# Performance work log

Measured on AMD Instinct MI355X. Metric: run time of the kernel, lower is better.

The kernel has to match this reference:

```python
import jax, jax.numpy as jnp
import numpy as np
from jax import lax

# Hardcoded module constants (from source)
T, B = 8, 64
CIN, C, HW, NCLS = 3, 64, 32, 10
V_INIT, V_DECAY, V_THR = 0.0, 0.8, 1.2


def conv_raw(x, w, b):
    # x: [T, B, Cin, H, W] -> conv2d per timestep, stride 1, pad 1
    t, bsz = x.shape[:2]
    xf = x.reshape((t * bsz,) + x.shape[2:])
    y = lax.conv_general_dilated(
        xf, w, window_strides=(1, 1), padding=[(1, 1), (1, 1)],
        dimension_numbers=('NCHW', 'OIHW', 'NCHW'))
    y = y + b[None, :, None, None]
    return y.reshape((t, bsz) + y.shape[1:])


def lif(i_cur):
    # NOTE: original code reads v[t] from the v_init-initialized tensor each
    # step (not v[t-1]), so there is NO temporal recurrence: v = v_init*decay + I[t]
    v = V_INIT * V_DECAY + i_cur
    return (v >= V_THR).astype(i_cur.dtype)


def setup_inputs() -> dict:
    key = jax.random.key(0)
    ks = jax.random.split(key, 7)
    spike_input = jax.random.uniform(ks[0], (T, B, CIN, HW, HW), jnp.float32)
    # original uses plain torch.randn for weights and biases
    w1 = jax.random.normal(ks[1], (C, CIN, 3, 3), jnp.float32)
    b1 = jax.random.normal(ks[2], (C,), jnp.float32)
    w2 = jax.random.normal(ks[3], (C, C, 3, 3), jnp.float32)
    b2 = jax.random.normal(ks[4], (C,), jnp.float32)
    wfc = jax.random.normal(ks[5], (NCLS, C * HW * HW), jnp.float32)
    bfc = jax.random.normal(ks[6], (NCLS,), jnp.float32)
    return {"spike_input": spike_input, "w1": w1, "b1": b1,
            "w2": w2, "b2": b2, "wfc": wfc, "bfc": bfc}


def reference(spike_input, w1, b1, w2, b2, wfc, bfc):
    x = lif(conv_raw(spike_input, w1, b1))      # [T,B,64,32,32] binary spikes
    x = lif(conv_raw(x, w2, b2))                # [T,B,64,32,32]
    x = x.reshape(T, B, -1)                     # [T,B,64*32*32]
    out = jnp.einsum('tbi,oi->tbo', x, wfc) + bfc
    return out.sum(0)                           # [B, 10]
```

## Files before the change

### kernel.cpp

```cpp
#include <hip/hip_runtime.h>
#include <hip/hip_bf16.h>


typedef __attribute__((ext_vector_type(8))) short bf16x8;
typedef __attribute__((ext_vector_type(4))) float f32x4;
typedef __attribute__((ext_vector_type(4))) int   i32x4;

#define S1Q (5.5f/127.0f)
#define S2Q (S1Q/254.0f)

static const size_t SZ_IMG  = 65536;
static const size_t OFF_S8  = 0;
static const size_t OFF_CNT = 512*SZ_IMG;
static const size_t OFF_W1F = OFF_CNT + (4u<<20);
static const size_t OFF_BQ  = OFF_W1F + 8192;

#define SWZ(cp) (((cp) >> 1) & 3)

__device__ __forceinline__ void gl_lds16(const void* g, void* l) {
  __builtin_amdgcn_global_load_lds(
      (const __attribute__((address_space(1))) unsigned int*)g,
      (__attribute__((address_space(3))) unsigned int*)l, 16, 0, 0);
}

__global__ __launch_bounds__(256) void kprep(
    const float* __restrict__ w1, const float* __restrict__ w2,
    short* __restrict__ W1F, signed char* __restrict__ Bq, float* __restrict__ out)
{
  int i = blockIdx.x*256 + threadIdx.x;
  if (i < 640) out[i] = 0.f;
  if (i < 4096) {
    int t2 = i >> 11, r = i & 2047, co = r >> 5, k = r & 31;
    short o = 0;
    if (k < 27) {
      int s = k/3, ci = k - s*3;
      float w = w1[co*27 + ci*9 + s];
      __hip_bfloat16 h = __float2bfloat16(w);
      if (t2 == 0) o = *(short*)&h;
      else { __hip_bfloat16 lo = __float2bfloat16(w - (float)h); o = *(short*)&lo; }
    }
    W1F[i] = o;
  }
  if (i < 36864) {
    int co = i/576, rem = i - co*576, ci = rem/9, s = rem - ci*9;
    float w = w2[i];
    int q1 = (int)roundf(w * (1.0f/S1Q)); q1 = q1 > 127 ? 127 : (q1 < -127 ? -127 : q1);
    float r1 = w - S1Q*(float)q1;
    int q2 = (int)roundf(r1 * (1.0f/S2Q)); q2 = q2 > 127 ? 127 : (q2 < -127 ? -127 : q2);
    int off = s*4096 + co*64 + ci;
    Bq[off] = (signed char)q1; Bq[36864 + off] = (signed char)q2;
  }
}

__global__ __launch_bounds__(256, 4) void conv1_k(
    const float* __restrict__ x, const short* __restrict__ W1F,
    const float* __restrict__ b1, unsigned char* __restrict__ S8)
{
  const int j   = blockIdx.x;
  const int img = j & 511, rh = j >> 9;
  const int tid = threadIdx.x;
  const int w   = tid >> 6;
  const int l   = tid & 63;
  const int lm  = l & 15, lk = l >> 4;

  __shared__ int xt4[1944];
  __shared__ i32x4 bnc4[4][16][4];
  unsigned short* xs = (unsigned short*)xt4;
  unsigned char*  bnc = (unsigned char*)bnc4;

  for (int i = tid; i < 1944; i += 256) xt4[i] = 0;
  __syncthreads();
  const float* xin = x + (size_t)img * 3072;
  for (int jj = tid; jj < 1728; jj += 256) {
    int ci = jj / 576, rem = jj - ci*576, rl = rem >> 5, c = rem & 31;
    int gr = rh*16 - 1 + rl;
    float f = (gr >= 0 && gr < 32) ? xin[ci*1024 + gr*32 + c] : 0.f;
    __hip_bfloat16 h = __float2bfloat16(f);
    __hip_bfloat16 lo = __float2bfloat16(f - (float)h);
    int idx = ci*648 + rl*36 + (c+1);
    xs[idx] = *(unsigned short*)&h;
    xs[idx + 1944] = *(unsigned short*)&lo;
  }
  __syncthreads();

  bf16x8 Wf[2][4];
  float  b1v[4];
  #pragma unroll
  for (int t2 = 0; t2 < 2; t2++)
    #pragma unroll
    for (int nf = 0; nf < 4; nf++)
      Wf[t2][nf] = *(const bf16x8*)(W1F + t2*2048 + (nf*16+lm)*32 + lk*8);
  #pragma unroll
  for (int nf = 0; nf < 4; nf++) b1v[nf] = b1[nf*16 + lm];

  int off16[8];
  #pragma unroll
  for (int e = 0; e < 8; e++) {
    int k = lk*8 + e;
    if (k < 27) { int s = k/3, ci = k - s*3, dr = s/3, dc = s - dr*3;
                  off16[e] = ci*648 + dr*36 + dc; }
    else off16[e] = 0;
  }

  unsigned char* S8b = S8 + (size_t)img * SZ_IMG;
  for (int fi = 0; fi < 8; fi++) {
    const int pxF = w*8 + fi;
    const int lrow = pxF >> 1, colh = pxF & 1;
    const int base16 = lrow*36 + colh*16 + lm;
    bf16x8 ah, al;
    #pragma unroll
    for (int e = 0; e < 8; e++) {
      int idx = base16 + off16[e];
      ah[e] = (short)xs[idx];
      al[e] = (short)xs[idx + 1944];
    }
    f32x4 acc[4] = {};
    #pragma unroll
    for (int nf = 0; nf < 4; nf++) {
      acc[nf] = __builtin_amdgcn_mfma_f32_16x16x32_bf16(ah, Wf[0][nf], acc[nf], 0,0,0);
      acc[nf] = __builtin_amdgcn_mfma_f32_16x16x32_bf16(al, Wf[0][nf], acc[nf], 0,0,0);
      acc[nf] = __builtin_amdgcn_mfma_f32_16x16x32_bf16(ah, Wf[1][nf], acc[nf], 0,0,0);
      acc[nf] = __builtin_amdgcn_mfma_f32_16x16x32_bf16(al, Wf[1][nf], acc[nf], 0,0,0);
    }
    #pragma unroll
    for (int nf = 0; nf < 4; nf++)
      #pragma unroll
      for (int e4 = 0; e4 < 4; e4++) {
        float v = acc[nf][e4] + b1v[nf];
        bnc[w*1024 + (lk*4+e4)*64 + nf*16 + lm] = (v >= 1.2f) ? 1 : 0;
      }
    const int pxl = l >> 2, coq = l & 3;
    i32x4 sp = *(const i32x4*)(bnc + w*1024 + pxl*64 + coq*16);
    const int gcol = colh*16 + pxl;
    const int grow = rh*16 + lrow;
    const int cq = coq ^ SWZ(gcol + 1);
    *(i32x4*)(S8b + (size_t)(grow*32 + gcol)*64 + cq*16) = sp;
  }
}

__global__ __launch_bounds__(512, 2) void conv2_k(
    const unsigned char* __restrict__ S8, const signed char* __restrict__ Bq,
    const float* __restrict__ b2, unsigned char* __restrict__ cnt)
{
  extern __shared__ __align__(16) unsigned char lds[];
  unsigned char* Abuf = lds;
  unsigned char* Blds = lds + 43520;

  const int j  = blockIdx.x;
  const int b  = j & 63;
  const int rs = (j >> 6) & 3;
  const int ch = j >> 8;
  const int tid = threadIdx.x;
  const int wv = tid >> 6, l = tid & 63;
  const int lm = l & 15, lk = l >> 4;
  const int rp = wv >> 1;
  const int cq = wv & 1;
  const int colocal = cq*16 + lm;

  const float b2v = b2[ch*32 + colocal];

  {
    i32x4 z = {0,0,0,0};
    i32x4* ap = (i32x4*)Abuf;
    for (int c = tid; c < 2720; c += 512) ap[c] = z;
  }
  __syncthreads();

  {
    const signed char* Bsrc = Bq;
    #pragma unroll
    for (int it = 0; it < 5; it++) {
      const int c = it*512 + tid;
      if (c < 2304) {
        const int q = c / 1152, r = c - q*1152, s = r >> 7, r2 = r & 127;
        const int col = r2 >> 2, cic = r2 & 3;
        gl_lds16(Bsrc + q*36864 + s*4096 + (ch*32+col)*64 + cic*16, Blds + c*16);
      }
    }
    const unsigned char* Simg = S8 + (size_t)b*SZ_IMG;
    #pragma unroll
    for (int it = 0; it < 3; it++) {
      const int c = it*512 + tid;
      if (c < 1280) {
        const int row = c >> 7, grow = rs*8 - 1 + row;
        if (grow >= 0 && grow < 32)
          gl_lds16(Simg + grow*2048 + (c&127)*16, Abuf + row*2176 + 64 + (c&127)*16);
      }
    }
  }
  __syncthreads();

  unsigned int cntp[4] = {};

  for (int t = 0; t < 8; t++) {
    if (t < 7) {
      const unsigned char* Simg = S8 + (size_t)((t+1)*64 + b)*SZ_IMG;
      unsigned char* bufn = Abuf + ((t+1) & 1)*21760;
      #pragma unroll
      for (int it = 0; it < 3; it++) {
        const int c = it*512 + tid;
        if (c < 1280) {
          const int row = c >> 7, grow = rs*8 - 1 + row;
          if (grow >= 0 && grow < 32)
            gl_lds16(Simg + grow*2048 + (c&127)*16, bufn + row*2176 + 64 + (c&127)*16);
        }
      }
    }

    const unsigned char* ab = Abuf + (t & 1)*21760;
    i32x4 acc1[4] = {}, acc2[4] = {};
    __builtin_amdgcn_s_setprio(1);
    #pragma unroll
    for (int s = 0; s < 9; s++) {
      const int dr = s/3, dc = s - dr*3;
      i32x4 Bf1 = *(const i32x4*)(Blds + s*2048 + colocal*64 + lk*16);
      i32x4 Bf2 = *(const i32x4*)(Blds + 18432 + s*2048 + colocal*64 + lk*16);
      #pragma unroll
      for (int a = 0; a < 4; a++) {
        const int lr = rp*2 + (a>>1) + dr;
        const int cp = ((a&1)<<4) + lm + dc;
        i32x4 Af = *(const i32x4*)(ab + lr*2176 + cp*64 + ((lk ^ SWZ(cp)) << 4));
        acc1[a] = __builtin_amdgcn_mfma_i32_16x16x64_i8(Af, Bf1, acc1[a], 0,0,0);
        acc2[a] = __builtin_amdgcn_mfma_i32_16x16x64_i8(Af, Bf2, acc2[a], 0,0,0);
      }
    }
    __builtin_amdgcn_s_setprio(0);

    #pragma unroll
    for (int a = 0; a < 4; a++) {
      unsigned int p = 0;
      #pragma unroll
      for (int e = 0; e < 4; e++) {
        float v = S1Q*(float)acc1[a][e] + S2Q*(float)acc2[a][e] + b2v;
        p |= (v >= 1.2f ? 1u : 0u) << (8*e);
      }
      cntp[a] += p;
    }
    __syncthreads();
  }

  unsigned int* bb = (unsigned int*)Abuf;
  #pragma unroll
  for (int a = 0; a < 4; a++) {
    const int lrow = rp*2 + (a>>1);
    const int u = lrow*8 + (a&1)*4 + lk;
    bb[colocal*64 + (((u>>2) ^ (colocal & 15)) << 2) + (u&3)] = cntp[a];
  }
  __syncthreads();
  {
    const int co = tid >> 4, tc = tid & 15;
    i32x4 v = *(const i32x4*)(bb + co*64 + (tc << 2));
    const int g = tc ^ (co & 15);
    *(i32x4*)(cnt + (size_t)(b*64 + ch*32 + co)*1024 + rs*256 + g*16) = v;
  }
}

__global__ __launch_bounds__(256) void fc_k(
    const unsigned char* __restrict__ cnt, const float* __restrict__ wfc,
    const float* __restrict__ bfc, float* __restrict__ out)
{
  const int ig = blockIdx.x & 63;
  const int bg = blockIdx.x >> 6;
  const int tid = threadIdx.x;
  const int w = tid >> 6, l = tid & 63;
  const int b0 = bg*8 + w*2;

  float acc[2][10] = {};
  #pragma unroll
  for (int k = 0; k < 4; k++) {
    const int i4 = ig*256 + k*64 + l;
    float4 wv[10];
    #pragma unroll
    for (int o = 0; o < 10; o++)
      wv[o] = *(const float4*)(wfc + (size_t)o*65536 + (size_t)i4*4);
    #pragma unroll
    for (int bb = 0; bb < 2; bb++) {
      uchar4 cv = *(const uchar4*)(cnt + (size_t)(b0+bb)*65536 + (size_t)i4*4);
      float c0 = cv.x, c1 = cv.y, c2 = cv.z, c3 = cv.w;
      #pragma unroll
      for (int o = 0; o < 10; o++)
        acc[bb][o] += wv[o].x*c0 + wv[o].y*c1 + wv[o].z*c2 + wv[o].w*c3;
    }
  }
  #pragma unroll
  for (int bb = 0; bb < 2; bb++)
    #pragma unroll
    for (int o = 0; o < 10; o++) {
      float v = acc[bb][o];
      for (int off = 32; off > 0; off >>= 1) v += __shfl_down(v, off, 64);
      acc[bb][o] = v;
    }
  if (l == 0) {
    #pragma unroll
    for (int bb = 0; bb < 2; bb++)
      #pragma unroll
      for (int o = 0; o < 10; o++) {
        float v = acc[bb][o];
        if (ig == 0) v += 8.0f * bfc[o];
        atomicAdd(out + (b0+bb)*10 + o, v);
      }
  }
}

extern "C" void kernel_launch(void* const* d_in, const int* in_sizes, int n_in,
                              void* d_out, int out_size, void* d_ws, size_t ws_size,
                              hipStream_t stream)
{
  const float* x   = (const float*)d_in[0];
  const float* w1  = (const float*)d_in[1];
  const float* b1  = (const float*)d_in[2];
  const float* w2  = (const float*)d_in[3];
  const float* b2  = (const float*)d_in[4];
  const float* wfc = (const float*)d_in[5];
  const float* bfc = (const float*)d_in[6];
  float* out = (float*)d_out;

  unsigned char* ws  = (unsigned char*)d_ws;
  unsigned char* S8  = ws + OFF_S8;
  unsigned char* cnt = ws + OFF_CNT;
  short*         W1F = (short*)(ws + OFF_W1F);
  signed char*   Bq  = (signed char*)(ws + OFF_BQ);

  kprep<<<144, 256, 0, stream>>>(w1, w2, W1F, Bq, out);
  conv1_k<<<1024, 256, 0, stream>>>(x, W1F, b1, S8);
  conv2_k<<<512, 512, 80384, stream>>>(S8, Bq, b2, cnt);
  fc_k<<<512, 256, 0, stream>>>(cnt, wfc, bfc, out);
}
```

Measured before the change: 146.1 us.

## Fuse FC into conv2 epilogue and compute conv1 weight split in-kernel

The FC layer is folded into the conv2 kernel's epilogue. Each block multiplies its spike-count tile by the matching wfc slice, reduces through shuffles and LDS, and atomically adds into the output, so the cnt buffer round trip and the separate fc launch go away. The conv1 bf16 hi/lo weight split now happens inside conv1 instead of in the prep kernel, and the bias is written into out during prep. In exchange, wfc is re-read per block with less batch reuse and there are more atomics per output element.

New measurement: 136.2 us. -6.7%, faster.

```diff
diff --git a/kernel.cpp b/kernel.cpp
--- a/kernel.cpp
+++ b/kernel.cpp
@@ -11,9 +11,7 @@
 
 static const size_t SZ_IMG  = 65536;
 static const size_t OFF_S8  = 0;
-static const size_t OFF_CNT = 512*SZ_IMG;
-static const size_t OFF_W1F = OFF_CNT + (4u<<20);
-static const size_t OFF_BQ  = OFF_W1F + 8192;
+static const size_t OFF_BQ  = 512*SZ_IMG;
 
 #define SWZ(cp) (((cp) >> 1) & 3)
 
@@ -24,23 +22,11 @@
 }
 
 __global__ __launch_bounds__(256) void kprep(
-    const float* __restrict__ w1, const float* __restrict__ w2,
-    short* __restrict__ W1F, signed char* __restrict__ Bq, float* __restrict__ out)
+    const float* __restrict__ w2, const float* __restrict__ bfc,
+    signed char* __restrict__ Bq, float* __restrict__ out)
 {
   int i = blockIdx.x*256 + threadIdx.x;
-  if (i < 640) out[i] = 0.f;
-  if (i < 4096) {
-    int t2 = i >> 11, r = i & 2047, co = r >> 5, k = r & 31;
-    short o = 0;
-    if (k < 27) {
-      int s = k/3, ci = k - s*3;
-      float w = w1[co*27 + ci*9 + s];
-      __hip_bfloat16 h = __float2bfloat16(w);
-      if (t2 == 0) o = *(short*)&h;
-      else { __hip_bfloat16 lo = __float2bfloat16(w - (float)h); o = *(short*)&lo; }
-    }
-    W1F[i] = o;
-  }
+  if (i < 640) out[i] = 8.0f * bfc[i % 10];
   if (i < 36864) {
     int co = i/576, rem = i - co*576, ci = rem/9, s = rem - ci*9;
     float w = w2[i];
@@ -53,7 +39,7 @@
 }
 
 __global__ __launch_bounds__(256, 4) void conv1_k(
-    const float* __restrict__ x, const short* __restrict__ W1F,
+    const float* __restrict__ x, const float* __restrict__ w1,
     const float* __restrict__ b1, unsigned char* __restrict__ S8)
 {
   const int j   = blockIdx.x;
@@ -81,26 +67,28 @@
     xs[idx] = *(unsigned short*)&h;
     xs[idx + 1944] = *(unsigned short*)&lo;
   }
-  __syncthreads();
 
   bf16x8 Wf[2][4];
   float  b1v[4];
-  #pragma unroll
-  for (int t2 = 0; t2 < 2; t2++)
-    #pragma unroll
-    for (int nf = 0; nf < 4; nf++)
-      Wf[t2][nf] = *(const bf16x8*)(W1F + t2*2048 + (nf*16+lm)*32 + lk*8);
-  #pragma unroll
-  for (int nf = 0; nf < 4; nf++) b1v[nf] = b1[nf*16 + lm];
-
   int off16[8];
   #pragma unroll
   for (int e = 0; e < 8; e++) {
     int k = lk*8 + e;
-    if (k < 27) { int s = k/3, ci = k - s*3, dr = s/3, dc = s - dr*3;
-                  off16[e] = ci*648 + dr*36 + dc; }
+    int s = k/3, ci = k - s*3;
+    if (k < 27) { int dr = s/3, dc = s - dr*3; off16[e] = ci*648 + dr*36 + dc; }
     else off16[e] = 0;
-  }
+    #pragma unroll
+    for (int nf = 0; nf < 4; nf++) {
+      float wv = (k < 27) ? w1[(nf*16+lm)*27 + ci*9 + s] : 0.f;
+      __hip_bfloat16 h = __float2bfloat16(wv);
+      __hip_bfloat16 lo = __float2bfloat16(wv - (float)h);
+      Wf[0][nf][e] = *(short*)&h;
+      Wf[1][nf][e] = *(short*)&lo;
+    }
+  }
+  #pragma unroll
+  for (int nf = 0; nf < 4; nf++) b1v[nf] = b1[nf*16 + lm];
+  __syncthreads();
 
   unsigned char* S8b = S8 + (size_t)img * SZ_IMG;
   for (int fi = 0; fi < 8; fi++) {
@@ -138,9 +126,10 @@
   }
 }
 
-__global__ __launch_bounds__(512, 2) void conv2_k(
+__global__ __launch_bounds__(512, 2) void conv2fc_k(
     const unsigned char* __restrict__ S8, const signed char* __restrict__ Bq,
-    const float* __restrict__ b2, unsigned char* __restrict__ cnt)
+    const float* __restrict__ b2, const float* __restrict__ wfc,
+    float* __restrict__ out)
 {
   extern __shared__ __align__(16) unsigned char lds[];
   unsigned char* Abuf = lds;
@@ -247,58 +236,44 @@
     bb[colocal*64 + (((u>>2) ^ (colocal & 15)) << 2) + (u&3)] = cntp[a];
   }
   __syncthreads();
+
+  float facc[10];
   {
-    const int co = tid >> 4, tc = tid & 15;
-    i32x4 v = *(const i32x4*)(bb + co*64 + (tc << 2));
-    const int g = tc ^ (co & 15);
-    *(i32x4*)(cnt + (size_t)(b*64 + ch*32 + co)*1024 + rs*256 + g*16) = v;
-  }
-}
-
-__global__ __launch_bounds__(256) void fc_k(
-    const unsigned char* __restrict__ cnt, const float* __restrict__ wfc,
-    const float* __restrict__ bfc, float* __restrict__ out)
-{
-  const int ig = blockIdx.x & 63;
-  const int bg = blockIdx.x >> 6;
-  const int tid = threadIdx.x;
-  const int w = tid >> 6, l = tid & 63;
-  const int b0 = bg*8 + w*2;
-
-  float acc[2][10] = {};
+    const int co = tid >> 4, seg = tid & 15;
+    i32x4 cw = *(const i32x4*)(bb + co*64 + ((seg ^ (co & 15)) << 2));
+    const unsigned char* cb = (const unsigned char*)&cw;
+    const size_t ibase = (size_t)(ch*32 + co)*1024 + rs*256 + seg*16;
+    #pragma unroll
+    for (int o = 0; o < 10; o++) {
+      const float* wp = wfc + (size_t)o*65536 + ibase;
+      float s0 = 0.f;
+      #pragma unroll
+      for (int q4 = 0; q4 < 4; q4++) {
+        float4 wv4 = *(const float4*)(wp + q4*4);
+        s0 += wv4.x*(float)cb[q4*4+0] + wv4.y*(float)cb[q4*4+1]
+            + wv4.z*(float)cb[q4*4+2] + wv4.w*(float)cb[q4*4+3];
+      }
+      facc[o] = s0;
+    }
+  }
   #pragma unroll
-  for (int k = 0; k < 4; k++) {
-    const int i4 = ig*256 + k*64 + l;
-    float4 wv[10];
-    #pragma unroll
-    for (int o = 0; o < 10; o++)
-      wv[o] = *(const float4*)(wfc + (size_t)o*65536 + (size_t)i4*4);
-    #pragma unroll
-    for (int bb = 0; bb < 2; bb++) {
-      uchar4 cv = *(const uchar4*)(cnt + (size_t)(b0+bb)*65536 + (size_t)i4*4);
-      float c0 = cv.x, c1 = cv.y, c2 = cv.z, c3 = cv.w;
-      #pragma unroll
-      for (int o = 0; o < 10; o++)
-        acc[bb][o] += wv[o].x*c0 + wv[o].y*c1 + wv[o].z*c2 + wv[o].w*c3;
-    }
-  }
-  #pragma unroll
-  for (int bb = 0; bb < 2; bb++)
-    #pragma unroll
-    for (int o = 0; o < 10; o++) {
-      float v = acc[bb][o];
-      for (int off = 32; off > 0; off >>= 1) v += __shfl_down(v, off, 64);
-      acc[bb][o] = v;
-    }
+  for (int o = 0; o < 10; o++) {
+    float v = facc[o];
+    #pragma unroll
+    for (int off = 32; off > 0; off >>= 1) v += __shfl_down(v, off, 64);
+    facc[o] = v;
+  }
+  float* red = (float*)(Abuf + 16384);
   if (l == 0) {
     #pragma unroll
-    for (int bb = 0; bb < 2; bb++)
-      #pragma unroll
-      for (int o = 0; o < 10; o++) {
-        float v = acc[bb][o];
-        if (ig == 0) v += 8.0f * bfc[o];
-        atomicAdd(out + (b0+bb)*10 + o, v);
-      }
+    for (int o = 0; o < 10; o++) red[wv*10 + o] = facc[o];
+  }
+  __syncthreads();
+  if (tid < 10) {
+    float v = 0.f;
+    #pragma unroll
+    for (int q = 0; q < 8; q++) v += red[q*10 + tid];
+    atomicAdd(out + b*10 + tid, v);
   }
 }
 
@@ -317,12 +292,9 @@
 
   unsigned char* ws  = (unsigned char*)d_ws;
   unsigned char* S8  = ws + OFF_S8;
-  unsigned char* cnt = ws + OFF_CNT;
-  short*         W1F = (short*)(ws + OFF_W1F);
   signed char*   Bq  = (signed char*)(ws + OFF_BQ);
 
-  kprep<<<144, 256, 0, stream>>>(w1, w2, W1F, Bq, out);
-  conv1_k<<<1024, 256, 0, stream>>>(x, W1F, b1, S8);
-  conv2_k<<<512, 512, 80384, stream>>>(S8, Bq, b2, cnt);
-  fc_k<<<512, 256, 0, stream>>>(cnt, wfc, bfc, out);
-}
+  kprep<<<144, 256, 0, stream>>>(w2, bfc, Bq, out);
+  conv1_k<<<1024, 256, 0, stream>>>(x, w1, b1, S8);
+  conv2fc_k<<<512, 512, 80384, stream>>>(S8, Bq, b2, wfc, out);
+}
```
